# Performance work log

Hardware: AMD Instinct MI355X
Metric: run time of the kernel (lower is better)

## Reference

```python
import jax, jax.numpy as jnp
import numpy as np

N, E, IN, H, OUT, L = 20000, 320000, 256, 256, 128, 3
EPS = 1e-5


def setup_inputs() -> dict:
    key = jax.random.key(0)
    ks = jax.random.split(key, 16)
    s = 0.02
    return {
        "x": jax.random.normal(ks[0], (N, IN), jnp.float32),
        "edge_index": jax.random.randint(ks[1], (2, E), 0, N, jnp.int64),
        "in_w": jax.random.normal(ks[2], (IN, H), jnp.float32) * s,
        "in_b": jnp.zeros((H,), jnp.float32),
        "parent_w": jax.random.normal(ks[3], (L, H, H), jnp.float32) * s,
        "child_w": jax.random.normal(ks[4], (L, H, H), jnp.float32) * s,
        "self_w": jax.random.normal(ks[5], (L, H, H), jnp.float32) * s,
        "self_b": jnp.zeros((L, H), jnp.float32),
        "ln_g": jnp.ones((L, H), jnp.float32),
        "ln_b": jnp.zeros((L, H), jnp.float32),
        "head_w1": jax.random.normal(ks[6], (H, H), jnp.float32) * s,
        "head_b1": jnp.zeros((H,), jnp.float32),
        "head_w2": jax.random.normal(ks[7], (H, OUT), jnp.float32) * s,
        "head_b2": jnp.zeros((OUT,), jnp.float32),
    }


def _aggregate(h, src, dst, weight):
    # gather -> matmul -> scatter-add -> degree-normalize
    transformed = h[src] @ weight                       # [E, H]
    agg = jax.ops.segment_sum(transformed, dst, num_segments=N)
    deg = jax.ops.segment_sum(jnp.ones((src.shape[0],), h.dtype), dst, num_segments=N)
    deg = jnp.maximum(deg, 1.0)
    return agg / deg[:, None]


def _layer_norm(x, g, b):
    mu = jnp.mean(x, axis=-1, keepdims=True)
    var = jnp.mean(jnp.square(x - mu), axis=-1, keepdims=True)
    return (x - mu) * jax.lax.rsqrt(var + EPS) * g + b


def reference(x, edge_index, in_w, in_b, parent_w, child_w, self_w, self_b,
              ln_g, ln_b, head_w1, head_b1, head_w2, head_b2):
    src, dst = edge_index[0], edge_index[1]
    h = x @ in_w + in_b                                  # input_proj
    for l in range(L):
        parent_msg = _aggregate(h, src, dst, parent_w[l])
        child_msg = _aggregate(h, dst, src, child_w[l])  # reversed edges
        out = h @ self_w[l] + self_b[l] + parent_msg + child_msg
        out = jax.nn.gelu(out, approximate=False)
        # dropout is identity in eval mode (training=False)
        h = _layer_norm(h + out, ln_g[l], ln_b[l])
    y = jax.nn.gelu(h @ head_w1 + head_b1, approximate=False)
    return y @ head_w2 + head_b2
```

## Files before the change

### kernel.cpp

```cpp
#include <hip/hip_runtime.h>


#define H 256
#define LAYERS 3
#define OUTD 128
#define LN_EPS 1e-5f

typedef short s16x8 __attribute__((ext_vector_type(8)));
typedef unsigned short u16x4 __attribute__((ext_vector_type(4)));
typedef unsigned short u16x8 __attribute__((ext_vector_type(8)));
typedef float f32x4 __attribute__((ext_vector_type(4)));
typedef int i32x4 __attribute__((ext_vector_type(4)));

__device__ __forceinline__ unsigned short f2bf(float f) {
  unsigned int u = __float_as_uint(f);
  u += 0x7FFFu + ((u >> 16) & 1u);
  return (unsigned short)(u >> 16);
}
__device__ __forceinline__ float bf2f(unsigned short s) {
  return __uint_as_float(((unsigned int)s) << 16);
}
__device__ __forceinline__ float gelu_f(float x) {
  return 0.5f * x * (1.0f + erff(x * 0.70710678118654752440f));
}
__device__ __forceinline__ void gload16(const void* g, void* l) {
  __builtin_amdgcn_global_load_lds((const __attribute__((address_space(1))) void*)g,
                                   (__attribute__((address_space(3))) void*)l, 16, 0, 0);
}


__device__ __forceinline__ void store_split8(unsigned short* __restrict__ T, int NS, int sec,
                                             int row, int l, u16x4 hv, u16x4 lv) {
  size_t tb = ((size_t)((row >> 4) * NS + sec) << 4) + (l >> 3);
  int off = (((row & 15) + (((l >> 1) & 3) << 4)) << 3) + ((l & 1) << 2);
  *(u16x4*)(T + tb * 512 + off) = hv;
  *(u16x4*)(T + (tb + 8) * 512 + off) = lv;
}

__global__ void split_tiles_kernel(const float* __restrict__ X,
                                   unsigned short* __restrict__ T, int NS,
                                   unsigned short* __restrict__ Hc, int M)
{
  const int rb = blockIdx.x;
  const int l = threadIdx.x & 63;
  const int cq = threadIdx.x >> 6;
  const int row = (rb << 4) + (l & 15);
  if (row >= M) return;
  const float* xr = X + (size_t)row * H;
#pragma unroll
  for (int p = 0; p < 2; ++p) {
    const int c = cq + (p << 2);
    const int j0 = (c << 5) + ((l >> 4) << 3);
    f32x4 v0 = *(const f32x4*)(xr + j0);
    f32x4 v1 = *(const f32x4*)(xr + j0 + 4);
    u16x8 hv, lv;
#pragma unroll
    for (int i = 0; i < 4; ++i) {
      unsigned short hb = f2bf(v0[i]); hv[i] = hb;     lv[i] = f2bf(v0[i] - bf2f(hb));
      unsigned short hc = f2bf(v1[i]); hv[4 + i] = hc; lv[4 + i] = f2bf(v1[i] - bf2f(hc));
    }
    size_t tb = ((size_t)(rb * NS) << 4);
    *(u16x8*)(T + (tb + c) * 512 + (l << 3)) = hv;
    *(u16x8*)(T + (tb + c + 8) * 512 + (l << 3)) = lv;
    if (Hc) *(u16x8*)(Hc + (size_t)row * H + j0) = hv;
  }
}

__global__ void bext_all_kernel(const float* __restrict__ in_w,
                                const float* __restrict__ parent_w,
                                const float* __restrict__ child_w,
                                const float* __restrict__ self_w,
                                const float* __restrict__ head_w1,
                                const float* __restrict__ head_w2,
                                unsigned short* __restrict__ Bext)
{
  const int slot = blockIdx.x >> 8;
  const int chunk = blockIdx.x & 255;
  const int ncol = (slot == 11) ? OUTD : H;
  const int idx = chunk * 256 + threadIdx.x;
  if (idx >= H * ncol) return;
  const float* W =
    (slot == 0)  ? in_w :
    (slot <= 3)  ? parent_w + (size_t)(slot - 1) * H * H :
    (slot <= 6)  ? child_w  + (size_t)(slot - 4) * H * H :
    (slot <= 9)  ? self_w   + (size_t)(slot - 7) * H * H :
    (slot == 10) ? head_w1  : head_w2;
  unsigned short* Bt = Bext + (size_t)slot * H * 512;
  int k = idx / ncol;
  int n = idx - k * ncol;
  float w = W[idx];
  unsigned short hb = f2bf(w);
  unsigned short lb = f2bf(w - bf2f(hb));
  size_t base = (((size_t)(n >> 4) << 4) + (k >> 5)) * 512 +
                (((n & 15) + (((k >> 3) & 3) << 4)) << 3) + (k & 7);
  Bt[base] = hb;
  Bt[base + 8 * 512] = lb;
}

__global__ void zero2_kernel(int* __restrict__ a, int* __restrict__ b, int n) {
  int i = blockIdx.x * 256 + threadIdx.x;
  if (i < n) { a[i] = 0; b[i] = 0; }
}

__global__ void deg_kernel(const int* __restrict__ src, const int* __restrict__ dst,
                           int* __restrict__ di, int* __restrict__ dox, int E) {
  int e = blockIdx.x * 256 + threadIdx.x;
  if (e >= E) return;
  atomicAdd(&dox[src[e]], 1);
  atomicAdd(&di[dst[e]], 1);
}

__global__ void rdeg_kernel(const int* __restrict__ di, const int* __restrict__ dox,
                            float* __restrict__ ri, float* __restrict__ ro,
                            int* __restrict__ cur_in, int* __restrict__ cur_out, int n) {
  int i = blockIdx.x * 256 + threadIdx.x;
  if (i >= n) return;
  int a = di[i];  if (a < 1) a = 1;
  int b = dox[i]; if (b < 1) b = 1;
  ri[i] = 1.0f / (float)a;
  ro[i] = 1.0f / (float)b;
  cur_in[i] = 0;
  cur_out[i] = 0;
}

__global__ __launch_bounds__(1024)
void scan2_kernel(const int* __restrict__ degi, const int* __restrict__ dego,
                  int* __restrict__ rp_in, int* __restrict__ rp_out, int n) {
  __shared__ int partial[1024];
  const int* deg = blockIdx.x ? dego : degi;
  int* rowptr = blockIdx.x ? rp_out : rp_in;
  const int t = threadIdx.x;
  const int chunk = (n + 1023) / 1024;
  int b = t * chunk;
  int e = b + chunk; if (e > n) e = n;
  int s = 0;
  for (int i = b; i < e; ++i) s += deg[i];
  partial[t] = s;
  __syncthreads();
  for (int off = 1; off < 1024; off <<= 1) {
    int v = (t >= off) ? partial[t - off] : 0;
    __syncthreads();
    partial[t] += v;
    __syncthreads();
  }
  int run = (t == 0) ? 0 : partial[t - 1];
  for (int i = b; i < e; ++i) { rowptr[i] = run; run += deg[i]; }
  if (t == 1023) rowptr[n] = run;
}

__global__ void fill_kernel(const int* __restrict__ src, const int* __restrict__ dst,
                            const int* __restrict__ rp_in, const int* __restrict__ rp_out,
                            int* __restrict__ cur_in, int* __restrict__ cur_out,
                            int* __restrict__ ci_in, int* __restrict__ ci_out, int E) {
  int e = blockIdx.x * 256 + threadIdx.x;
  if (e >= E) return;
  int s = src[e], d = dst[e];
  int p = atomicAdd(&cur_in[d], 1);
  ci_in[rp_in[d] + p] = s;
  int q = atomicAdd(&cur_out[s], 1);
  ci_out[rp_out[s] + q] = d;
}

template<int NF>
__global__ __launch_bounds__(256)
void gemm_kernel(const unsigned short* __restrict__ A, int NSa,
                 const unsigned short* __restrict__ B0,
                 const unsigned short* __restrict__ B1,
                 const unsigned short* __restrict__ B2,
                 const float* __restrict__ bias, float* __restrict__ C,
                 int M, int nrb, int nsec, int do_gelu)
{
  constexpr int N = NF * 64;
  __shared__ unsigned short ldsA[2][2048];

  const int tid = threadIdx.x;
  const int lane = tid & 63;
  const int wn = tid >> 6;
  const int m0 = blockIdx.x << 5;
  int rbw = (blockIdx.x << 1) + (wn & 1);
  if (rbw >= nrb) rbw = nrb - 1;
  const int hilo = wn >> 1;

  f32x4 acc[2][NF] = {};

  auto STAGE = [&](int buf, int step) {
    const int s = step >> 3;
    const int c = step & 7;
    const unsigned short* pa =
        A + (((size_t)(rbw * NSa + s) << 4) + c + (hilo << 3)) * 512 + (lane << 3);
    gload16(pa, &ldsA[buf][0] + (wn << 9));
  };

  auto COMPUTE = [&](int buf, int step) {
    const int s = step >> 3;
    const int c = step & 7;
    const unsigned short* Bs = (s == 0) ? B0 : ((s == 1) ? B1 : B2);
    s16x8 bh[NF], bl[NF];
#pragma unroll
    for (int j = 0; j < NF; ++j) {
      const int g = wn * NF + j;
      bh[j] = *(const s16x8*)(Bs + ((size_t)((g << 4) + c) << 9) + (lane << 3));
      bl[j] = *(const s16x8*)(Bs + ((size_t)((g << 4) + c + 8) << 9) + (lane << 3));
    }
    const unsigned short* base = &ldsA[buf][0];
    s16x8 ah[2], al[2];
#pragma unroll
    for (int f = 0; f < 2; ++f) {
      ah[f] = *(const s16x8*)(base + (f << 9) + (lane << 3));
      al[f] = *(const s16x8*)(base + 1024 + (f << 9) + (lane << 3));
    }
#pragma unroll
    for (int i = 0; i < 2; ++i)
#pragma unroll
      for (int j = 0; j < NF; ++j)
        acc[i][j] = __builtin_amdgcn_mfma_f32_16x16x32_bf16(ah[i], bh[j], acc[i][j], 0, 0, 0);
#pragma unroll
    for (int i = 0; i < 2; ++i)
#pragma unroll
      for (int j = 0; j < NF; ++j)
        acc[i][j] = __builtin_amdgcn_mfma_f32_16x16x32_bf16(ah[i], bl[j], acc[i][j], 0, 0, 0);
#pragma unroll
    for (int i = 0; i < 2; ++i)
#pragma unroll
      for (int j = 0; j < NF; ++j)
        acc[i][j] = __builtin_amdgcn_mfma_f32_16x16x32_bf16(al[i], bh[j], acc[i][j], 0, 0, 0);
  };

  const int nsteps = nsec << 3;
  STAGE(0, 0);
  int cur = 0;
  for (int t = 0; t < nsteps - 1; ++t) {
    STAGE(cur ^ 1, t + 1);
    asm volatile("s_waitcnt vmcnt(1)" ::: "memory");
    __builtin_amdgcn_s_barrier();
    COMPUTE(cur, t);
    asm volatile("s_waitcnt lgkmcnt(0)" ::: "memory");
    __builtin_amdgcn_s_barrier();
    cur ^= 1;
  }
  asm volatile("s_waitcnt vmcnt(0)" ::: "memory");
  __builtin_amdgcn_s_barrier();
  COMPUTE(cur, nsteps - 1);

  const int r0 = (lane >> 4) << 2;
  const int cn = lane & 15;
#pragma unroll
  for (int j = 0; j < NF; ++j) {
    const int col = wn * (NF << 4) + (j << 4) + cn;
    const float bb = bias ? bias[col] : 0.0f;
#pragma unroll
    for (int i = 0; i < 2; ++i) {
      const int rowb = m0 + (i << 4) + r0;
#pragma unroll
      for (int r = 0; r < 4; ++r) {
        const int rr = rowb + r;
        if (rr < M) {
          float v = acc[i][j][r] + bb;
          if (do_gelu) v = gelu_f(v);
          C[(size_t)rr * N + col] = v;
        }
      }
    }
  }
}

__device__ __forceinline__ void gacc8(const int* __restrict__ ci, int beg, int end,
                                      const unsigned short* __restrict__ Hc, int foff,
                                      float* __restrict__ acc) {
  int i = beg;
  for (; i < end && (i & 3); ++i) {
    u16x8 a = *(const u16x8*)(Hc + ((size_t)ci[i] << 8) + foff);
#pragma unroll
    for (int z = 0; z < 8; ++z) acc[z] += bf2f(a[z]);
  }
  for (; i + 4 <= end; i += 4) {
    i32x4 id = *(const i32x4*)(ci + i);
    u16x8 a = *(const u16x8*)(Hc + ((size_t)id[0] << 8) + foff);
    u16x8 b = *(const u16x8*)(Hc + ((size_t)id[1] << 8) + foff);
    u16x8 c = *(const u16x8*)(Hc + ((size_t)id[2] << 8) + foff);
    u16x8 d = *(const u16x8*)(Hc + ((size_t)id[3] << 8) + foff);
#pragma unroll
    for (int z = 0; z < 8; ++z)
      acc[z] += (bf2f(a[z]) + bf2f(b[z])) + (bf2f(c[z]) + bf2f(d[z]));
  }
  for (; i < end; ++i) {
    u16x8 a = *(const u16x8*)(Hc + ((size_t)ci[i] << 8) + foff);
#pragma unroll
    for (int z = 0; z < 8; ++z) acc[z] += bf2f(a[z]);
  }
}

__global__ __launch_bounds__(256)
void gather_kernel(
    const int* __restrict__ rp_in, const int* __restrict__ ci_in,
    const int* __restrict__ rp_out, const int* __restrict__ ci_out,
    const float* __restrict__ ri, const float* __restrict__ ro,
    const unsigned short* __restrict__ Hc, unsigned short* __restrict__ Aext,
    int M, int nrb, int npair)
{
  __shared__ unsigned short sh[2][2][2][2][512];
  const int b = blockIdx.x;
  const int xcd = b & 7;
  const int s = xcd >> 1;
  const int rbp = ((b >> 3) << 1) + (xcd & 1);
  if (rbp >= npair) return;
  const int tid = threadIdx.x;
  const int g = tid >> 3;
  const int t = tid & 7;
  const int row = (rbp << 5) + g;
  const int foff = (s << 6) + (t << 3);

  float hin[8] = {}, hout[8] = {};
  float wi = 0.f, wo = 0.f;
  if (row < M) {
    gacc8(ci_in,  rp_in[row],  rp_in[row + 1],  Hc, foff, hin);
    gacc8(ci_out, rp_out[row], rp_out[row + 1], Hc, foff, hout);
    wi = ri[row];
    wo = ro[row];
  }

  const int rbl = g >> 4;
  const int cc = t >> 2;
  const int pos = ((g & 15) << 3) + ((t & 3) << 7);
  u16x8 hv, lv;
#pragma unroll
  for (int q = 0; q < 8; ++q) {
    float v = hin[q] * wi;
    unsigned short hb = f2bf(v);
    hv[q] = hb; lv[q] = f2bf(v - bf2f(hb));
  }
  *(u16x8*)(&sh[rbl][0][0][cc][pos]) = hv;
  *(u16x8*)(&sh[rbl][0][1][cc][pos]) = lv;
#pragma unroll
  for (int q = 0; q < 8; ++q) {
    float v = hout[q] * wo;
    unsigned short hb = f2bf(v);
    hv[q] = hb; lv[q] = f2bf(v - bf2f(hb));
  }
  *(u16x8*)(&sh[rbl][1][0][cc][pos]) = hv;
  *(u16x8*)(&sh[rbl][1][1][cc][pos]) = lv;
  __syncthreads();

  const int tp = tid >> 4;
  const int q = tid & 15;
  const int rbl2 = tp >> 3, sec = (tp >> 2) & 1, hilo = (tp >> 1) & 1, c2 = tp & 1;
  const int rb = (rbp << 1) + rbl2;
  if (rb < nrb) {
    const int cg = (s << 1) + c2 + (hilo << 3);
    size_t tile = ((size_t)(rb * 3 + 1 + sec) << 4) + cg;
    unsigned short* dstp = Aext + tile * 512;
    const unsigned short* srcp = &sh[rbl2][sec][hilo][c2][0];
#pragma unroll
    for (int i = 0; i < 4; ++i)
      *(u16x8*)(dstp + (i << 7) + (q << 3)) = *(const u16x8*)(srcp + (i << 7) + (q << 3));
  }
}

__global__ void finalize_kernel(float* __restrict__ h, const float* __restrict__ P,
                                unsigned short* __restrict__ Aext,
                                unsigned short* __restrict__ Hc,
                                const float* __restrict__ g, const float* __restrict__ b, int M)
{
  int row = blockIdx.x * 4 + (threadIdx.x >> 6);
  if (row >= M) return;
  int l = threadIdx.x & 63;
  int j = l << 2;
  f32x4 hv = *(const f32x4*)(h + (size_t)row * H + j);
  f32x4 pv = *(const f32x4*)(P + (size_t)row * H + j);
  f32x4 t;
  float sum = 0.f, sq = 0.f;
#pragma unroll
  for (int i = 0; i < 4; ++i) {
    t[i] = hv[i] + gelu_f(pv[i]);
    sum += t[i];
    sq += t[i] * t[i];
  }
#pragma unroll
  for (int off = 1; off < 64; off <<= 1) {
    sum += __shfl_xor(sum, off, 64);
    sq  += __shfl_xor(sq, off, 64);
  }
  float mu = sum * (1.0f / H);
  float var = sq * (1.0f / H) - mu * mu;
  float rs = rsqrtf(var + LN_EPS);
  f32x4 outv;
  u16x4 hvv, lvv;
#pragma unroll
  for (int i = 0; i < 4; ++i) {
    outv[i] = (t[i] - mu) * rs * g[j + i] + b[j + i];
    unsigned short hb = f2bf(outv[i]);
    hvv[i] = hb;
    lvv[i] = f2bf(outv[i] - bf2f(hb));
  }
  *(f32x4*)(h + (size_t)row * H + j) = outv;
  *(u16x4*)(Hc + ((size_t)row << 8) + j) = hvv;
  store_split8(Aext, 3, 0, row, l, hvv, lvv);
}

extern "C" void kernel_launch(void* const* d_in, const int* in_sizes, int n_in,
                              void* d_out, int out_size, void* d_ws, size_t ws_size,
                              hipStream_t stream)
{
  const float* x        = (const float*)d_in[0];
  const int*   ei       = (const int*)d_in[1];
  const float* in_w     = (const float*)d_in[2];
  const float* in_b     = (const float*)d_in[3];
  const float* parent_w = (const float*)d_in[4];
  const float* child_w  = (const float*)d_in[5];
  const float* self_w   = (const float*)d_in[6];
  const float* self_b   = (const float*)d_in[7];
  const float* ln_g     = (const float*)d_in[8];
  const float* ln_b     = (const float*)d_in[9];
  const float* head_w1  = (const float*)d_in[10];
  const float* head_b1  = (const float*)d_in[11];
  const float* head_w2  = (const float*)d_in[12];
  const float* head_b2  = (const float*)d_in[13];

  const int M = in_sizes[0] / H;
  const int E = in_sizes[1] / 2;
  const int nrb = (M + 15) / 16;
  const int npair = (nrb + 1) / 2;
  const int* src = ei;
  const int* dst = ei + E;

  char* w = (char*)d_ws;
  auto alloc = [&](size_t bytes) { char* p = w; w += (bytes + 255) & ~(size_t)255; return p; };
  float*          h    = (float*)alloc((size_t)M * H * 4);
  float*          P    = (float*)alloc((size_t)M * H * 4);
  unsigned short* Ax   = (unsigned short*)alloc((size_t)nrb * 16 * 512 * 2);
  unsigned short* Aext = (unsigned short*)alloc((size_t)nrb * 48 * 512 * 2);
  unsigned short* Hc   = (unsigned short*)alloc((size_t)M * H * 2);
  unsigned short* Bext = (unsigned short*)alloc((size_t)12 * H * 512 * 2);
  int*            degi = (int*)alloc((size_t)M * 4);
  int*            dego = (int*)alloc((size_t)M * 4);
  float*          ri   = (float*)alloc((size_t)M * 4);
  float*          ro   = (float*)alloc((size_t)M * 4);
  int*            rp_in   = (int*)alloc((size_t)(M + 1) * 4);
  int*            rp_out  = (int*)alloc((size_t)(M + 1) * 4);
  int*            cur_in  = (int*)alloc((size_t)M * 4);
  int*            cur_out = (int*)alloc((size_t)M * 4);
  int*            ci_in   = (int*)alloc((size_t)E * 4);
  int*            ci_out  = (int*)alloc((size_t)E * 4);
  if ((size_t)(w - (char*)d_ws) > ws_size) return;

  auto bslot = [&](int i) { return Bext + (size_t)i * H * 512; };

  bext_all_kernel<<<12 * 256, 256, 0, stream>>>(in_w, parent_w, child_w, self_w,
                                                head_w1, head_w2, Bext);

  zero2_kernel<<<(M + 255) / 256, 256, 0, stream>>>(degi, dego, M);
  deg_kernel<<<(E + 255) / 256, 256, 0, stream>>>(src, dst, degi, dego, E);
  rdeg_kernel<<<(M + 255) / 256, 256, 0, stream>>>(degi, dego, ri, ro, cur_in, cur_out, M);
  scan2_kernel<<<2, 1024, 0, stream>>>(degi, dego, rp_in, rp_out, M);
  fill_kernel<<<(E + 255) / 256, 256, 0, stream>>>(src, dst, rp_in, rp_out,
                                                   cur_in, cur_out, ci_in, ci_out, E);

  const int mb32 = (M + 31) / 32;
  const int ggrid = (M + 3) / 4;
  const int xgrid = 8 * ((npair + 1) / 2);

  split_tiles_kernel<<<nrb, 256, 0, stream>>>(x, Ax, 1, nullptr, M);
  gemm_kernel<4><<<mb32, 256, 0, stream>>>(Ax, 1, bslot(0), nullptr, nullptr,
                                           in_b, h, M, nrb, 1, 0);
  split_tiles_kernel<<<nrb, 256, 0, stream>>>(h, Aext, 3, Hc, M);

  for (int l = 0; l < LAYERS; ++l) {
    gather_kernel<<<xgrid, 256, 0, stream>>>(rp_in, ci_in, rp_out, ci_out,
                                             ri, ro, Hc, Aext, M, nrb, npair);
    gemm_kernel<4><<<mb32, 256, 0, stream>>>(Aext, 3,
                                             bslot(7 + l), bslot(1 + l), bslot(4 + l),
                                             self_b + (size_t)l * H, P, M, nrb, 3, 0);
    finalize_kernel<<<ggrid, 256, 0, stream>>>(h, P, Aext, Hc,
                                               ln_g + (size_t)l * H, ln_b + (size_t)l * H, M);
  }

  gemm_kernel<4><<<mb32, 256, 0, stream>>>(Aext, 3, bslot(10), nullptr, nullptr,
                                           head_b1, P, M, nrb, 1, 1);
  split_tiles_kernel<<<nrb, 256, 0, stream>>>(P, Ax, 1, nullptr, M);
  gemm_kernel<2><<<mb32, 256, 0, stream>>>(Ax, 1, bslot(11), nullptr, nullptr,
                                           head_b2, (float*)d_out, M, nrb, 1, 0);
}
```

Baseline: 456.9 us.

## Parallelize gather over edges with a wavefront per row and shuffle reduction

The gather kernel previously gave each row to 8 threads that walked the whole neighbor list serially. Now each row gets a full 64-lane wavefront: 8 lanes split the edges while 8 lanes cover the features, and partial sums are combined with xor shuffles. Blocks grow to 1024 threads and cover a single 16-row block instead of a pair. This exposes more memory-level parallelism for the random row gathers, at the cost of shuffle reductions, idle lanes on low-degree rows, and fewer rows per block.

```diff
diff --git a/kernel.cpp b/kernel.cpp
--- a/kernel.cpp
+++ b/kernel.cpp
@@ -10,7 +10,6 @@
 typedef unsigned short u16x4 __attribute__((ext_vector_type(4)));
 typedef unsigned short u16x8 __attribute__((ext_vector_type(8)));
 typedef float f32x4 __attribute__((ext_vector_type(4)));
-typedef int i32x4 __attribute__((ext_vector_type(4)));
 
 __device__ __forceinline__ unsigned short f2bf(float f) {
   unsigned int u = __float_as_uint(f);
@@ -264,95 +263,101 @@
   }
 }
 
-__device__ __forceinline__ void gacc8(const int* __restrict__ ci, int beg, int end,
-                                      const unsigned short* __restrict__ Hc, int foff,
-                                      float* __restrict__ acc) {
-  int i = beg;
-  for (; i < end && (i & 3); ++i) {
-    u16x8 a = *(const u16x8*)(Hc + ((size_t)ci[i] << 8) + foff);
-#pragma unroll
-    for (int z = 0; z < 8; ++z) acc[z] += bf2f(a[z]);
-  }
-  for (; i + 4 <= end; i += 4) {
-    i32x4 id = *(const i32x4*)(ci + i);
-    u16x8 a = *(const u16x8*)(Hc + ((size_t)id[0] << 8) + foff);
-    u16x8 b = *(const u16x8*)(Hc + ((size_t)id[1] << 8) + foff);
-    u16x8 c = *(const u16x8*)(Hc + ((size_t)id[2] << 8) + foff);
-    u16x8 d = *(const u16x8*)(Hc + ((size_t)id[3] << 8) + foff);
-#pragma unroll
-    for (int z = 0; z < 8; ++z)
-      acc[z] += (bf2f(a[z]) + bf2f(b[z])) + (bf2f(c[z]) + bf2f(d[z]));
-  }
-  for (; i < end; ++i) {
-    u16x8 a = *(const u16x8*)(Hc + ((size_t)ci[i] << 8) + foff);
-#pragma unroll
-    for (int z = 0; z < 8; ++z) acc[z] += bf2f(a[z]);
-  }
-}
-
-__global__ __launch_bounds__(256)
+__global__ __launch_bounds__(1024)
 void gather_kernel(
     const int* __restrict__ rp_in, const int* __restrict__ ci_in,
     const int* __restrict__ rp_out, const int* __restrict__ ci_out,
     const float* __restrict__ ri, const float* __restrict__ ro,
     const unsigned short* __restrict__ Hc, unsigned short* __restrict__ Aext,
-    int M, int nrb, int npair)
-{
-  __shared__ unsigned short sh[2][2][2][2][512];
+    int M, int nrb)
+{
+  __shared__ unsigned short sh[2][2][2][512];
   const int b = blockIdx.x;
   const int xcd = b & 7;
   const int s = xcd >> 1;
-  const int rbp = ((b >> 3) << 1) + (xcd & 1);
-  if (rbp >= npair) return;
+  const int rb = ((b >> 3) << 1) + (xcd & 1);
+  if (rb >= nrb) return;
   const int tid = threadIdx.x;
-  const int g = tid >> 3;
-  const int t = tid & 7;
-  const int row = (rbp << 5) + g;
-  const int foff = (s << 6) + (t << 3);
+  const int w = tid >> 6;
+  const int lane = tid & 63;
+  const int e = lane >> 3;
+  const int o = lane & 7;
+  const int row = (rb << 4) + w;
+  const int foff = (s << 6) + (o << 3);
 
   float hin[8] = {}, hout[8] = {};
   float wi = 0.f, wo = 0.f;
   if (row < M) {
-    gacc8(ci_in,  rp_in[row],  rp_in[row + 1],  Hc, foff, hin);
-    gacc8(ci_out, rp_out[row], rp_out[row + 1], Hc, foff, hout);
     wi = ri[row];
     wo = ro[row];
-  }
-
-  const int rbl = g >> 4;
-  const int cc = t >> 2;
-  const int pos = ((g & 15) << 3) + ((t & 3) << 7);
-  u16x8 hv, lv;
-#pragma unroll
-  for (int q = 0; q < 8; ++q) {
-    float v = hin[q] * wi;
-    unsigned short hb = f2bf(v);
-    hv[q] = hb; lv[q] = f2bf(v - bf2f(hb));
-  }
-  *(u16x8*)(&sh[rbl][0][0][cc][pos]) = hv;
-  *(u16x8*)(&sh[rbl][0][1][cc][pos]) = lv;
-#pragma unroll
-  for (int q = 0; q < 8; ++q) {
-    float v = hout[q] * wo;
-    unsigned short hb = f2bf(v);
-    hv[q] = hb; lv[q] = f2bf(v - bf2f(hb));
-  }
-  *(u16x8*)(&sh[rbl][1][0][cc][pos]) = hv;
-  *(u16x8*)(&sh[rbl][1][1][cc][pos]) = lv;
+#pragma unroll
+    for (int dir = 0; dir < 2; ++dir) {
+      const int* __restrict__ ci = dir ? ci_out : ci_in;
+      float* acc = dir ? hout : hin;
+      const int beg = dir ? rp_out[row] : rp_in[row];
+      const int end = dir ? rp_out[row + 1] : rp_in[row + 1];
+      int i0 = beg;
+      for (; i0 + 16 <= end; i0 += 16) {
+        int ia = ci[i0 + e];
+        int ib = ci[i0 + 8 + e];
+        u16x8 a = *(const u16x8*)(Hc + ((size_t)ia << 8) + foff);
+        u16x8 c = *(const u16x8*)(Hc + ((size_t)ib << 8) + foff);
+#pragma unroll
+        for (int z = 0; z < 8; ++z) acc[z] += bf2f(a[z]) + bf2f(c[z]);
+      }
+      for (; i0 < end; i0 += 8) {
+        int i = i0 + e;
+        if (i < end) {
+          int ia = ci[i];
+          u16x8 a = *(const u16x8*)(Hc + ((size_t)ia << 8) + foff);
+#pragma unroll
+          for (int z = 0; z < 8; ++z) acc[z] += bf2f(a[z]);
+        }
+      }
+    }
+#pragma unroll
+    for (int m = 8; m < 64; m <<= 1)
+#pragma unroll
+      for (int z = 0; z < 8; ++z) {
+        hin[z]  += __shfl_xor(hin[z], m, 64);
+        hout[z] += __shfl_xor(hout[z], m, 64);
+      }
+  }
+
+  if (lane < 8) {
+    const int cc = o >> 2;
+    const int pos = (w << 3) + ((o & 3) << 7);
+    u16x8 hv, lv;
+#pragma unroll
+    for (int q = 0; q < 8; ++q) {
+      float v = hin[q] * wi;
+      unsigned short hb = f2bf(v);
+      hv[q] = hb; lv[q] = f2bf(v - bf2f(hb));
+    }
+    *(u16x8*)(&sh[0][0][cc][pos]) = hv;
+    *(u16x8*)(&sh[0][1][cc][pos]) = lv;
+#pragma unroll
+    for (int q = 0; q < 8; ++q) {
+      float v = hout[q] * wo;
+      unsigned short hb = f2bf(v);
+      hv[q] = hb; lv[q] = f2bf(v - bf2f(hb));
+    }
+    *(u16x8*)(&sh[1][0][cc][pos]) = hv;
+    *(u16x8*)(&sh[1][1][cc][pos]) = lv;
+  }
   __syncthreads();
 
-  const int tp = tid >> 4;
-  const int q = tid & 15;
-  const int rbl2 = tp >> 3, sec = (tp >> 2) & 1, hilo = (tp >> 1) & 1, c2 = tp & 1;
-  const int rb = (rbp << 1) + rbl2;
-  if (rb < nrb) {
+  if (tid < 256) {
+    const int tp = tid >> 5;
+    const int q = tid & 31;
+    const int sec = tp >> 2, hilo = (tp >> 1) & 1, c2 = tp & 1;
     const int cg = (s << 1) + c2 + (hilo << 3);
     size_t tile = ((size_t)(rb * 3 + 1 + sec) << 4) + cg;
     unsigned short* dstp = Aext + tile * 512;
-    const unsigned short* srcp = &sh[rbl2][sec][hilo][c2][0];
-#pragma unroll
-    for (int i = 0; i < 4; ++i)
-      *(u16x8*)(dstp + (i << 7) + (q << 3)) = *(const u16x8*)(srcp + (i << 7) + (q << 3));
+    const unsigned short* srcp = &sh[sec][hilo][c2][0];
+#pragma unroll
+    for (int i = 0; i < 2; ++i)
+      *(u16x8*)(dstp + (i << 8) + (q << 3)) = *(const u16x8*)(srcp + (i << 8) + (q << 3));
   }
 }
 
@@ -419,7 +424,6 @@
   const int M = in_sizes[0] / H;
   const int E = in_sizes[1] / 2;
   const int nrb = (M + 15) / 16;
-  const int npair = (nrb + 1) / 2;
   const int* src = ei;
   const int* dst = ei + E;
 
@@ -457,7 +461,7 @@
 
   const int mb32 = (M + 31) / 32;
   const int ggrid = (M + 3) / 4;
-  const int xgrid = 8 * ((npair + 1) / 2);
+  const int xgrid = 8 * ((nrb + 1) / 2);
 
   split_tiles_kernel<<<nrb, 256, 0, stream>>>(x, Ax, 1, nullptr, M);
   gemm_kernel<4><<<mb32, 256, 0, stream>>>(Ax, 1, bslot(0), nullptr, nullptr,
@@ -465,8 +469,8 @@
   split_tiles_kernel<<<nrb, 256, 0, stream>>>(h, Aext, 3, Hc, M);
 
   for (int l = 0; l < LAYERS; ++l) {
-    gather_kernel<<<xgrid, 256, 0, stream>>>(rp_in, ci_in, rp_out, ci_out,
-                                             ri, ro, Hc, Aext, M, nrb, npair);
+    gather_kernel<<<xgrid, 1024, 0, stream>>>(rp_in, ci_in, rp_out, ci_out,
+                                              ri, ro, Hc, Aext, M, nrb);
     gemm_kernel<4><<<mb32, 256, 0, stream>>>(Aext, 3,
                                              bslot(7 + l), bslot(1 + l), bslot(4 + l),
                                              self_b + (size_t)l * H, P, M, nrb, 3, 0);
```

Result: slower. 531.0 us (+16.2%).

## Fuse bf16 split-tile packing into GEMM epilogue and shrink gather blocks

Applied to the files above, without the earlier changes.

The GEMM epilogue can now write the hi/lo bf16 split tiles (and the compact bf16 copy of h) directly. This removes the separate split_tiles_kernel launches after the input projection and the first head layer, and with them an fp32 round trip through global memory. The head-1 GEMM no longer writes its fp32 output at all. The gather kernel now handles one 16-row block per workgroup with 128 threads instead of a pair of blocks with 256, which doubles the grid. The new epilogue stores are scattered 2-byte writes, so they may coalesce poorly.

```diff
diff --git a/kernel.cpp b/kernel.cpp
--- a/kernel.cpp
+++ b/kernel.cpp
@@ -161,14 +161,16 @@
   ci_out[rp_out[s] + q] = d;
 }
 
-template<int NF>
+template<int NF, int GELU, int SPLIT>
 __global__ __launch_bounds__(256)
 void gemm_kernel(const unsigned short* __restrict__ A, int NSa,
                  const unsigned short* __restrict__ B0,
                  const unsigned short* __restrict__ B1,
                  const unsigned short* __restrict__ B2,
                  const float* __restrict__ bias, float* __restrict__ C,
-                 int M, int nrb, int nsec, int do_gelu)
+                 unsigned short* __restrict__ Asp, int NSp,
+                 unsigned short* __restrict__ Hc,
+                 int M, int nrb, int nsec)
 {
   constexpr int N = NF * 64;
   __shared__ unsigned short ldsA[2][2048];
@@ -256,8 +258,16 @@
         const int rr = rowb + r;
         if (rr < M) {
           float v = acc[i][j][r] + bb;
-          if (do_gelu) v = gelu_f(v);
-          C[(size_t)rr * N + col] = v;
+          if (GELU) v = gelu_f(v);
+          if (C) C[(size_t)rr * N + col] = v;
+          if (SPLIT) {
+            unsigned short hb = f2bf(v);
+            size_t tb = (((size_t)(rr >> 4) * NSp) << 4) + (col >> 5);
+            int off = ((rr & 15) << 3) + (((col >> 3) & 3) << 7) + (col & 7);
+            Asp[tb * 512 + off] = hb;
+            Asp[(tb + 8) * 512 + off] = f2bf(v - bf2f(hb));
+            if (Hc) Hc[((size_t)rr << 8) + col] = hb;
+          }
         }
       }
     }
@@ -290,24 +300,24 @@
   }
 }
 
-__global__ __launch_bounds__(256)
+__global__ __launch_bounds__(128)
 void gather_kernel(
     const int* __restrict__ rp_in, const int* __restrict__ ci_in,
     const int* __restrict__ rp_out, const int* __restrict__ ci_out,
     const float* __restrict__ ri, const float* __restrict__ ro,
     const unsigned short* __restrict__ Hc, unsigned short* __restrict__ Aext,
-    int M, int nrb, int npair)
-{
-  __shared__ unsigned short sh[2][2][2][2][512];
+    int M, int nrb)
+{
+  __shared__ unsigned short sh[2][2][2][512];
   const int b = blockIdx.x;
   const int xcd = b & 7;
   const int s = xcd >> 1;
-  const int rbp = ((b >> 3) << 1) + (xcd & 1);
-  if (rbp >= npair) return;
+  const int rb = ((b >> 3) << 1) + (xcd & 1);
+  if (rb >= nrb) return;
   const int tid = threadIdx.x;
   const int g = tid >> 3;
   const int t = tid & 7;
-  const int row = (rbp << 5) + g;
+  const int row = (rb << 4) + g;
   const int foff = (s << 6) + (t << 3);
 
   float hin[8] = {}, hout[8] = {};
@@ -319,9 +329,8 @@
     wo = ro[row];
   }
 
-  const int rbl = g >> 4;
   const int cc = t >> 2;
-  const int pos = ((g & 15) << 3) + ((t & 3) << 7);
+  const int pos = (g << 3) + ((t & 3) << 7);
   u16x8 hv, lv;
 #pragma unroll
   for (int q = 0; q < 8; ++q) {
@@ -329,31 +338,28 @@
     unsigned short hb = f2bf(v);
     hv[q] = hb; lv[q] = f2bf(v - bf2f(hb));
   }
-  *(u16x8*)(&sh[rbl][0][0][cc][pos]) = hv;
-  *(u16x8*)(&sh[rbl][0][1][cc][pos]) = lv;
+  *(u16x8*)(&sh[0][0][cc][pos]) = hv;
+  *(u16x8*)(&sh[0][1][cc][pos]) = lv;
 #pragma unroll
   for (int q = 0; q < 8; ++q) {
     float v = hout[q] * wo;
     unsigned short hb = f2bf(v);
     hv[q] = hb; lv[q] = f2bf(v - bf2f(hb));
   }
-  *(u16x8*)(&sh[rbl][1][0][cc][pos]) = hv;
-  *(u16x8*)(&sh[rbl][1][1][cc][pos]) = lv;
+  *(u16x8*)(&sh[1][0][cc][pos]) = hv;
+  *(u16x8*)(&sh[1][1][cc][pos]) = lv;
   __syncthreads();
 
   const int tp = tid >> 4;
   const int q = tid & 15;
-  const int rbl2 = tp >> 3, sec = (tp >> 2) & 1, hilo = (tp >> 1) & 1, c2 = tp & 1;
-  const int rb = (rbp << 1) + rbl2;
-  if (rb < nrb) {
-    const int cg = (s << 1) + c2 + (hilo << 3);
-    size_t tile = ((size_t)(rb * 3 + 1 + sec) << 4) + cg;
-    unsigned short* dstp = Aext + tile * 512;
-    const unsigned short* srcp = &sh[rbl2][sec][hilo][c2][0];
-#pragma unroll
-    for (int i = 0; i < 4; ++i)
-      *(u16x8*)(dstp + (i << 7) + (q << 3)) = *(const u16x8*)(srcp + (i << 7) + (q << 3));
-  }
+  const int sec = tp >> 2, hilo = (tp >> 1) & 1, c2 = tp & 1;
+  const int cg = (s << 1) + c2 + (hilo << 3);
+  size_t tile = ((size_t)(rb * 3 + 1 + sec) << 4) + cg;
+  unsigned short* dstp = Aext + tile * 512;
+  const unsigned short* srcp = &sh[sec][hilo][c2][0];
+#pragma unroll
+  for (int i = 0; i < 4; ++i)
+    *(u16x8*)(dstp + (i << 7) + (q << 3)) = *(const u16x8*)(srcp + (i << 7) + (q << 3));
 }
 
 __global__ void finalize_kernel(float* __restrict__ h, const float* __restrict__ P,
@@ -419,7 +425,6 @@
   const int M = in_sizes[0] / H;
   const int E = in_sizes[1] / 2;
   const int nrb = (M + 15) / 16;
-  const int npair = (nrb + 1) / 2;
   const int* src = ei;
   const int* dst = ei + E;
 
@@ -457,26 +462,26 @@
 
   const int mb32 = (M + 31) / 32;
   const int ggrid = (M + 3) / 4;
-  const int xgrid = 8 * ((npair + 1) / 2);
+  const int xgrid = 8 * ((nrb + 1) / 2);
 
   split_tiles_kernel<<<nrb, 256, 0, stream>>>(x, Ax, 1, nullptr, M);
-  gemm_kernel<4><<<mb32, 256, 0, stream>>>(Ax, 1, bslot(0), nullptr, nullptr,
-                                           in_b, h, M, nrb, 1, 0);
-  split_tiles_kernel<<<nrb, 256, 0, stream>>>(h, Aext, 3, Hc, M);
+  gemm_kernel<4, 0, 1><<<mb32, 256, 0, stream>>>(Ax, 1, bslot(0), nullptr, nullptr,
+                                                 in_b, h, Aext, 3, Hc, M, nrb, 1);
 
   for (int l = 0; l < LAYERS; ++l) {
-    gather_kernel<<<xgrid, 256, 0, stream>>>(rp_in, ci_in, rp_out, ci_out,
-                                             ri, ro, Hc, Aext, M, nrb, npair);
-    gemm_kernel<4><<<mb32, 256, 0, stream>>>(Aext, 3,
-                                             bslot(7 + l), bslot(1 + l), bslot(4 + l),
-                                             self_b + (size_t)l * H, P, M, nrb, 3, 0);
+    gather_kernel<<<xgrid, 128, 0, stream>>>(rp_in, ci_in, rp_out, ci_out,
+                                             ri, ro, Hc, Aext, M, nrb);
+    gemm_kernel<4, 0, 0><<<mb32, 256, 0, stream>>>(Aext, 3,
+                                                   bslot(7 + l), bslot(1 + l), bslot(4 + l),
+                                                   self_b + (size_t)l * H, P,
+                                                   nullptr, 0, nullptr, M, nrb, 3);
     finalize_kernel<<<ggrid, 256, 0, stream>>>(h, P, Aext, Hc,
                                                ln_g + (size_t)l * H, ln_b + (size_t)l * H, M);
   }
 
-  gemm_kernel<4><<<mb32, 256, 0, stream>>>(Aext, 3, bslot(10), nullptr, nullptr,
-                                           head_b1, P, M, nrb, 1, 1);
-  split_tiles_kernel<<<nrb, 256, 0, stream>>>(P, Ax, 1, nullptr, M);
-  gemm_kernel<2><<<mb32, 256, 0, stream>>>(Ax, 1, bslot(11), nullptr, nullptr,
-                                           head_b2, (float*)d_out, M, nrb, 1, 0);
-}
+  gemm_kernel<4, 1, 1><<<mb32, 256, 0, stream>>>(Aext, 3, bslot(10), nullptr, nullptr,
+                                                 head_b1, nullptr, Ax, 1, nullptr, M, nrb, 1);
+  gemm_kernel<2, 0, 0><<<mb32, 256, 0, stream>>>(Ax, 1, bslot(11), nullptr, nullptr,
+                                                 head_b2, (float*)d_out, nullptr, 0, nullptr,
+                                                 M, nrb, 1);
+}
```

New measurement: 441.5 us. 3.4% less time.
